# Kernel tuning notes

Hardware: AMD Instinct MI355X
Metric: run time of the kernel (lower is better)

## Reference

```python
import jax, jax.numpy as jnp
import numpy as np
import math

N_HEAD = 12
N_EMBD = 768

def setup_inputs() -> dict:
    key = jax.random.key(0)
    ks = jax.random.split(key, 5)
    B, T, C = 4, 2048, N_EMBD
    s_attn = 1.0 / math.sqrt(C)
    return {
        "x": jax.random.normal(ks[0], (B, T, C), jnp.float32),
        "w_attn": jax.random.normal(ks[1], (C, 3 * C), jnp.float32) * s_attn,
        "b_attn": jnp.zeros((3 * C,), jnp.float32),
        "w_proj": jax.random.normal(ks[2], (C, C), jnp.float32) * s_attn,
        "b_proj": jnp.zeros((C,), jnp.float32),
    }

def reference(x, w_attn, b_attn, w_proj, b_proj):
    B, T, C = x.shape
    H = N_HEAD
    D = C // H
    qkv = x @ w_attn + b_attn  # [B,T,3C]
    q, k, v = jnp.split(qkv, 3, axis=-1)
    # [B,T,C] -> [B,H,T,D]
    q = q.reshape(B, T, H, D).transpose(0, 2, 1, 3)
    k = k.reshape(B, T, H, D).transpose(0, 2, 1, 3)
    v = v.reshape(B, T, H, D).transpose(0, 2, 1, 3)
    att = jnp.einsum('bhqd,bhkd->bhqk', q, k) * (1.0 / math.sqrt(D))
    causal = jnp.tril(jnp.ones((T, T), bool))
    att = jnp.where(causal[None, None], att, -jnp.inf)
    att = jax.nn.softmax(att, axis=-1)
    y = jnp.einsum('bhqk,bhkd->bhqd', att, v)  # [B,H,T,D]
    y = y.transpose(0, 2, 1, 3).reshape(B, T, C)
    return y @ w_proj + b_proj
```

## Files before the change

kernel.cpp:

```cpp
#include <hip/hip_runtime.h>
#include <hip/hip_bf16.h>

typedef unsigned short u16;
typedef __attribute__((ext_vector_type(4))) short bf16x4;
typedef __attribute__((ext_vector_type(8))) short bf16x8;
typedef __attribute__((ext_vector_type(4))) float f32x4;
typedef __attribute__((ext_vector_type(16))) float f32x16;

#define NB_ 4
#define NT_ 2048
#define NC_ 768
#define NH_ 12
#define ND_ 64
#define NM_ (NB_*NT_)
#define KC_ 24

#define SCQ_ 0.18033688011112042f

__device__ __forceinline__ u16 f2bf(float f){
  union { float f; unsigned u; } c; c.f = f;
  unsigned u = c.u;
  return (u16)((u + 0x7fffu + ((u>>16)&1u)) >> 16);
}

__device__ __forceinline__ unsigned pkbf(float a, float b){
  __hip_bfloat162 h = __float22bfloat162_rn(make_float2(a,b));
  union { __hip_bfloat162 h; unsigned u; } c; c.h = h; return c.u;
}

__device__ __forceinline__ f32x16 mfma32(bf16x8 a, bf16x8 b, f32x16 c){
  return __builtin_amdgcn_mfma_f32_32x32x16_bf16(a, b, c, 0, 0, 0);
}

__device__ __forceinline__ void gload_lds16(const void* g, void* l){
  __builtin_amdgcn_global_load_lds(
    (const __attribute__((address_space(1))) void*)g,
    (__attribute__((address_space(3))) void*)l, 16, 0, 0);
}


__global__ __launch_bounds__(256) void cast_f32_bf16_k(
    const float* __restrict__ in, u16* __restrict__ out, int n4){
  int i = blockIdx.x*256 + threadIdx.x;
  if (i >= n4) return;
  float4 v = ((const float4*)in)[i];
  int row = i / (NC_/4), k4 = (i % (NC_/4))*4;
  size_t off = (((size_t)(row>>7)*KC_ + (k4>>5))*4 + ((k4>>3)&3))*1024 + (row&127)*8 + (k4&7);
  bf16x4 o;
  o[0]=(short)f2bf(v.x); o[1]=(short)f2bf(v.y);
  o[2]=(short)f2bf(v.z); o[3]=(short)f2bf(v.w);
  *(bf16x4*)(out + off) = o;
}

__global__ __launch_bounds__(256) void transpose_cast_k(
    const float* __restrict__ in, u16* __restrict__ out, int R, int Cc){
  __shared__ float tile[32][33];
  int tx = threadIdx.x, ty = threadIdx.y;
  int c0 = blockIdx.x*32, r0 = blockIdx.y*32;
  #pragma unroll
  for (int j=0;j<32;j+=8) tile[ty+j][tx] = in[(size_t)(r0+ty+j)*Cc + c0+tx];
  __syncthreads();
  #pragma unroll
  for (int j=0;j<32;j+=8){
    int n = c0+ty+j, k = r0+tx;
    size_t off = (((size_t)(n>>7)*KC_ + (k>>5))*4 + ((k>>3)&3))*1024 + (n&127)*8 + (k&7);
    out[off] = f2bf(tile[tx][ty+j]);
  }
}

template<int MODE>
__global__ __launch_bounds__(256,3) void gemm128p(
  const u16* __restrict__ A, const u16* __restrict__ BT, const float* __restrict__ bias,
  u16* __restrict__ qo, u16* __restrict__ ko, u16* __restrict__ vo,
  float* __restrict__ fo)
{
  __shared__ u16 lds[3][8192];
  const int t = threadIdx.x, w = t>>6, l = t&63;
  const int lq = l&31, h = l>>5;
  const int NXB = (MODE==0) ? 18 : 6;
  const int nwg = 64*NXB;
  int sw = (blockIdx.x & 7)*(nwg>>3) + (blockIdx.x >> 3);
  const int rb = sw / NXB, nb = sw % NXB;
  const int brow = rb*128, bcol = nb*128;
  const int wr = (w>>1)*64, wc = (w&1)*64;

  f32x16 acc[2][2];
  #pragma unroll
  for (int i=0;i<2;i++)
    #pragma unroll
    for (int j=0;j<2;j++)
      #pragma unroll
      for (int r=0;r<16;r++) acc[i][j][r] = 0.f;

  auto stage = [&](int buf, int kc){
    const u16* Ag = A  + ((size_t)(rb*KC_ + kc))*4096;
    const u16* Bg = BT + ((size_t)(nb*KC_ + kc))*4096;
    char* La = (char*)&lds[buf][0];
    char* Lb = (char*)&lds[buf][4096];
    #pragma unroll
    for (int it=0; it<2; ++it){
      gload_lds16(Ag + (it*256+t)*8, La + (it*256+t)*16);
      gload_lds16(Bg + (it*256+t)*8, Lb + (it*256+t)*16);
    }
  };

  stage(0,0);
  stage(1,1);
  int cur = 0;
  for (int kc=0; kc<KC_; ++kc){
    if (kc+1 < KC_) asm volatile("s_waitcnt vmcnt(4)\ns_barrier" ::: "memory");
    else            asm volatile("s_waitcnt vmcnt(0)\ns_barrier" ::: "memory");
    if (kc+2 < KC_){ int nb3 = cur+2; if (nb3>=3) nb3-=3; stage(nb3, kc+2); }
    const u16* La = &lds[cur][0];
    const u16* Lb = &lds[cur][4096];
    #pragma unroll
    for (int ks=0; ks<2; ++ks){
      bf16x8 af[2], bfr[2];
      #pragma unroll
      for (int mi=0;mi<2;mi++)
        af[mi]  = *(const bf16x8*)(La + ((2*ks+h)*128 + wr + mi*32 + lq)*8);
      #pragma unroll
      for (int nj=0;nj<2;nj++)
        bfr[nj] = *(const bf16x8*)(Lb + ((2*ks+h)*128 + wc + nj*32 + lq)*8);
      __builtin_amdgcn_s_setprio(1);
      #pragma unroll
      for (int mi=0;mi<2;mi++)
        #pragma unroll
        for (int nj=0;nj<2;nj++)
          acc[mi][nj] = mfma32(af[mi], bfr[nj], acc[mi][nj]);
      __builtin_amdgcn_s_setprio(0);
    }
    if (++cur == 3) cur = 0;
  }

  if (MODE == 1){
    #pragma unroll
    for (int nj=0;nj<2;nj++){
      int n = bcol + wc + nj*32 + lq;
      float bs = bias[n];
      #pragma unroll
      for (int mi=0;mi<2;mi++)
        #pragma unroll
        for (int r=0;r<16;r++){
          int m = brow + wr + mi*32 + (r&3) + 8*(r>>2) + 4*h;
          fo[(size_t)m*NC_ + n] = acc[mi][nj][r] + bs;
        }
    }
  } else {
    const int sec = nb/6;
    u16* outp = (sec==0) ? qo : (sec==1 ? ko : vo);
    #pragma unroll
    for (int nj=0;nj<2;nj++){
      int n = bcol + wc + nj*32 + lq;
      int cc = n - sec*NC_;
      int hd = cc >> 6, d = cc & 63;
      float bs = bias[n];
      #pragma unroll
      for (int mi=0;mi<2;mi++)
        #pragma unroll
        for (int r=0;r<16;r++){
          int m = brow + wr + mi*32 + (r&3) + 8*(r>>2) + 4*h;
          int bb = m >> 11, tt = m & 2047;
          float v = acc[mi][nj][r] + bs;
          if (sec == 0) v *= SCQ_;
          size_t bhbase = ((size_t)bb*NH_ + hd)*((size_t)NT_*ND_);
          size_t off;
          if (sec == 0){
            off = bhbase + (size_t)tt*ND_ + d;
          } else if (sec == 1){
            off = bhbase + (size_t)(tt>>6)*4096 + (size_t)(d>>3)*512 + (tt&63)*8 + (d&7);
          } else {
            int p = (tt & ~15) | (h<<3) | (r&3) | (((r>>2)&1)<<2);
            off = bhbase + (size_t)(p>>6)*4096 + (size_t)((p&63)>>3)*512 + d*8 + (p&7);
          }
          outp[off] = f2bf(v);
        }
    }
  }
}

__global__ __launch_bounds__(256,4) void attn_kernel(
    const u16* __restrict__ qg, const u16* __restrict__ kg,
    const u16* __restrict__ vg, u16* __restrict__ y)
{
  __shared__ u16 lds[2][8192];
  const int t = threadIdx.x, w = t>>6, l = t&63;
  const int lq = l&31, h = l>>5;
  const int bid = blockIdx.x;
  const int qt = 15 - (bid/48);
  const int bh = bid % 48;
  const int bb = bh / NH_, hh = bh % NH_;
  const u16* qp = qg + (size_t)bh*NT_*ND_;
  const u16* kp = kg + (size_t)bh*NT_*ND_;
  const u16* vp = vg + (size_t)bh*ND_*NT_;
  const int qmin = qt*128 + w*32;
  const int q = qmin + lq;

  bf16x8 Qf[4];
  {
    const u16* qr = qp + (size_t)q*ND_ + 8*h;
    #pragma unroll
    for (int ks=0; ks<4; ++ks) Qf[ks] = *(const bf16x8*)(qr + ks*16);
  }

  f32x16 o0, o1;
  float psum[16];
  #pragma unroll
  for (int r=0;r<16;r++){ o0[r]=0.f; o1[r]=0.f; psum[r]=0.f; }
  const int nc = 2*qt + 2;

  auto stage = [&](int buf, int c){
    const u16* kc2 = kp + c*4096;
    const u16* vc2 = vp + c*4096;
    #pragma unroll
    for (int it=0; it<2; ++it){
      gload_lds16(kc2 + (it*256 + t)*8, (char*)&lds[buf][0]    + (it*256 + t)*16);
      gload_lds16(vc2 + (it*256 + t)*8, (char*)&lds[buf][4096] + (it*256 + t)*16);
    }
  };

  stage(0,0);
  int cur = 0;
  for (int c=0; c<nc; ++c){
    asm volatile("s_waitcnt vmcnt(0)\ns_barrier" ::: "memory");
    if (c+1 < nc) stage(cur^1, c+1);

    const u16* Kb = &lds[cur][0];
    const u16* Vb = &lds[cur][4096];
    const int kv0 = c*64;

    f32x16 s0, s1;
    #pragma unroll
    for (int r=0;r<16;r++){ s0[r]=0.f; s1[r]=0.f; }
    __builtin_amdgcn_s_setprio(1);
    #pragma unroll
    for (int ks=0; ks<4; ++ks){
      bf16x8 k0 = *(const bf16x8*)(Kb + ((2*ks+h)*64      + lq)*8);
      bf16x8 k1 = *(const bf16x8*)(Kb + ((2*ks+h)*64 + 32 + lq)*8);
      s0 = mfma32(k0, Qf[ks], s0);
      s1 = mfma32(k1, Qf[ks], s1);
    }
    __builtin_amdgcn_s_setprio(0);

    if (kv0 + 63 > qmin){
      #pragma unroll
      for (int r=0;r<16;r++){
        int kva = kv0 + (r&3) + 8*(r>>2) + 4*h;
        s0[r] = (kva      <= q) ? s0[r] : -3e38f;
        s1[r] = (kva + 32 <= q) ? s1[r] : -3e38f;
      }
    }

    union { unsigned wd[16]; bf16x8 v[4]; } pf;
    #pragma unroll
    for (int j=0;j<8;j++){
      float a = exp2f(s0[2*j]), b = exp2f(s0[2*j+1]);
      psum[j] += a + b;
      pf.wd[j] = pkbf(a,b);
    }
    #pragma unroll
    for (int j=0;j<8;j++){
      float a = exp2f(s1[2*j]), b = exp2f(s1[2*j+1]);
      psum[8+j] += a + b;
      pf.wd[8+j] = pkbf(a,b);
    }

    __builtin_amdgcn_s_setprio(1);
    #pragma unroll
    for (int j=0;j<4;j++){
      bf16x8 v0 = *(const bf16x8*)(Vb + ((2*j+h)*64      + lq)*8);
      bf16x8 v1 = *(const bf16x8*)(Vb + ((2*j+h)*64 + 32 + lq)*8);
      o0 = mfma32(v0, pf.v[j], o0);
      o1 = mfma32(v1, pf.v[j], o1);
    }
    __builtin_amdgcn_s_setprio(0);
    cur ^= 1;
  }

  #pragma unroll
  for (int st=8; st>=1; st>>=1)
    #pragma unroll
    for (int i=0;i<st;i++) psum[i] += psum[i+st];
  float lsum = psum[0] + __shfl_xor(psum[0], 32);
  float inv = 1.f / lsum;

  const int m = bb*NT_ + q;
  const int rbm = m>>7, rr = m&127;
  #pragma unroll
  for (int db=0; db<2; ++db){
    #pragma unroll
    for (int g2=0; g2<4; ++g2){
      float e0 = (db ? o1[g2*4+0] : o0[g2*4+0]) * inv;
      float e1 = (db ? o1[g2*4+1] : o0[g2*4+1]) * inv;
      float e2 = (db ? o1[g2*4+2] : o0[g2*4+2]) * inv;
      float e3 = (db ? o1[g2*4+3] : o0[g2*4+3]) * inv;
      unsigned w0 = pkbf(e0,e1), w1 = pkbf(e2,e3);
      int k = hh*ND_ + db*32 + g2*8 + 4*h;
      size_t off = (((size_t)rbm*KC_ + (k>>5))*4 + ((k>>3)&3))*1024 + rr*8 + (k&7);
      *(uint2*)(y + off) = make_uint2(w0, w1);
    }
  }
}

extern "C" void kernel_launch(void* const* d_in, const int* in_sizes, int n_in,
                              void* d_out, int out_size, void* d_ws, size_t ws_size,
                              hipStream_t stream) {
  const float* x  = (const float*)d_in[0];
  const float* wa = (const float*)d_in[1];
  const float* ba = (const float*)d_in[2];
  const float* wp = (const float*)d_in[3];
  const float* bp = (const float*)d_in[4];
  float* out = (float*)d_out;

  char* ws = (char*)d_ws;
  const size_t szXB = (size_t)NM_*NC_*2;
  const size_t szWA = (size_t)3*NC_*NC_*2;
  const size_t szWP = (size_t)NC_*NC_*2;
  const size_t szQ  = szXB;
  u16* xb  = (u16*)(ws);
  u16* wat = (u16*)(ws + szXB);
  u16* wpt = (u16*)(ws + szXB + szWA);
  u16* qb  = (u16*)(ws + szXB + szWA + szWP);
  u16* kb  = (u16*)((char*)qb + szQ);
  u16* vb  = (u16*)((char*)kb + szQ);
  u16* yb  = xb;

  cast_f32_bf16_k<<<dim3((NM_*NC_/4 + 255)/256), dim3(256), 0, stream>>>(x, xb, NM_*NC_/4);
  transpose_cast_k<<<dim3(3*NC_/32, NC_/32), dim3(32,8), 0, stream>>>(wa, wat, NC_, 3*NC_);
  transpose_cast_k<<<dim3(NC_/32, NC_/32), dim3(32,8), 0, stream>>>(wp, wpt, NC_, NC_);
  gemm128p<0><<<dim3(64*18), dim3(256), 0, stream>>>(xb, wat, ba, qb, kb, vb, (float*)nullptr);
  attn_kernel<<<dim3(NB_*NH_*(NT_/128)), dim3(256), 0, stream>>>(qb, kb, vb, yb);
  gemm128p<1><<<dim3(64*6), dim3(256), 0, stream>>>(yb, wpt, bp,
      (u16*)nullptr, (u16*)nullptr, (u16*)nullptr, out);
}
```

Before: 132.9 us.

## Retile QKV GEMM to 256x96, double-buffer GEMMs, skip masked attention chunks

The QKV projection GEMM now uses 256x96 tiles (768 workgroups, one per CU-friendly grid) with a matching 96-wide weight panel layout, and both GEMMs move from triple to double buffering. The attention kernel skips fully masked KV chunks per wave and computes the softmax row sum with an extra MFMA against a ones vector instead of scalar adds plus shuffles. Together these aim to improve tile reuse and wave balance, cut wasted causal work, and trim VALU pressure, at the cost of less prefetch depth in the GEMMs and one extra MFMA per chunk in attention.

```diff
diff --git a/kernel.cpp b/kernel.cpp
--- a/kernel.cpp
+++ b/kernel.cpp
@@ -4,7 +4,6 @@
 typedef unsigned short u16;
 typedef __attribute__((ext_vector_type(4))) short bf16x4;
 typedef __attribute__((ext_vector_type(8))) short bf16x8;
-typedef __attribute__((ext_vector_type(4))) float f32x4;
 typedef __attribute__((ext_vector_type(16))) float f32x16;
 
 #define NB_ 4
@@ -52,6 +51,7 @@
   *(bf16x4*)(out + off) = o;
 }
 
+template<int PAN>
 __global__ __launch_bounds__(256) void transpose_cast_k(
     const float* __restrict__ in, u16* __restrict__ out, int R, int Cc){
   __shared__ float tile[32][33];
@@ -63,24 +63,112 @@
   #pragma unroll
   for (int j=0;j<32;j+=8){
     int n = c0+ty+j, k = r0+tx;
-    size_t off = (((size_t)(n>>7)*KC_ + (k>>5))*4 + ((k>>3)&3))*1024 + (n&127)*8 + (k&7);
+    size_t off = ((size_t)(n/PAN)*KC_ + (k>>5))*(PAN*32)
+               + (size_t)((k>>3)&3)*(PAN*8) + (n%PAN)*8 + (k&7);
     out[off] = f2bf(tile[tx][ty+j]);
   }
 }
 
-template<int MODE>
-__global__ __launch_bounds__(256,3) void gemm128p(
+__global__ __launch_bounds__(256,3) void gemmQ(
   const u16* __restrict__ A, const u16* __restrict__ BT, const float* __restrict__ bias,
-  u16* __restrict__ qo, u16* __restrict__ ko, u16* __restrict__ vo,
+  u16* __restrict__ qo, u16* __restrict__ ko, u16* __restrict__ vo)
+{
+  __shared__ u16 lds[2][11264];
+  const int t = threadIdx.x, w = t>>6, l = t&63;
+  const int lq = l&31, h = l>>5;
+  int sw = (blockIdx.x & 7)*96 + (blockIdx.x >> 3);
+  const int rb = sw / 24, nb = sw % 24;
+  const int brow = rb*256, bcol = nb*96;
+
+  f32x16 acc[2][3];
+  #pragma unroll
+  for (int i=0;i<2;i++)
+    #pragma unroll
+    for (int j=0;j<3;j++)
+      #pragma unroll
+      for (int r=0;r<16;r++) acc[i][j][r] = 0.f;
+
+  auto stage = [&](int buf, int kc){
+    const u16* A0 = A  + ((size_t)((rb*2  )*KC_ + kc))*4096;
+    const u16* A1 = A  + ((size_t)((rb*2+1)*KC_ + kc))*4096;
+    const u16* Bg = BT + ((size_t)(nb*KC_ + kc))*3072;
+    char* L = (char*)&lds[buf][0];
+    gload_lds16(A0 + t*8,         L + t*16);
+    gload_lds16(A0 + (256+t)*8,   L + (256+t)*16);
+    gload_lds16(A1 + t*8,         L + 8192  + t*16);
+    gload_lds16(A1 + (256+t)*8,   L + 8192  + (256+t)*16);
+    gload_lds16(Bg + t*8,         L + 16384 + t*16);
+    if (t < 128)
+      gload_lds16(Bg + (256+t)*8, L + 16384 + (256+t)*16);
+  };
+
+  stage(0,0);
+  int cur = 0;
+  for (int kc=0; kc<KC_; ++kc){
+    asm volatile("s_waitcnt vmcnt(0)\ns_barrier" ::: "memory");
+    if (kc+1 < KC_) stage(cur^1, kc+1);
+    const u16* La = &lds[cur][(w>>1)*4096];
+    const u16* Lb = &lds[cur][8192];
+    #pragma unroll
+    for (int ks=0; ks<2; ++ks){
+      bf16x8 af[2], bfr[3];
+      #pragma unroll
+      for (int mi=0;mi<2;mi++)
+        af[mi]  = *(const bf16x8*)(La + ((2*ks+h)*128 + (w&1)*64 + mi*32 + lq)*8);
+      #pragma unroll
+      for (int nj=0;nj<3;nj++)
+        bfr[nj] = *(const bf16x8*)(Lb + ((2*ks+h)*96 + nj*32 + lq)*8);
+      __builtin_amdgcn_s_setprio(1);
+      #pragma unroll
+      for (int mi=0;mi<2;mi++)
+        #pragma unroll
+        for (int nj=0;nj<3;nj++)
+          acc[mi][nj] = mfma32(af[mi], bfr[nj], acc[mi][nj]);
+      __builtin_amdgcn_s_setprio(0);
+    }
+    cur ^= 1;
+  }
+
+  const int sec = nb >> 3;
+  u16* outp = (sec==0) ? qo : (sec==1 ? ko : vo);
+  #pragma unroll
+  for (int nj=0;nj<3;nj++){
+    int n = bcol + nj*32 + lq;
+    int cc = n - sec*NC_;
+    int hd = cc >> 6, d = cc & 63;
+    float bs = bias[n];
+    #pragma unroll
+    for (int mi=0;mi<2;mi++)
+      #pragma unroll
+      for (int r=0;r<16;r++){
+        int m = brow + w*64 + mi*32 + (r&3) + 8*(r>>2) + 4*h;
+        int bb = m >> 11, tt = m & 2047;
+        float v = acc[mi][nj][r] + bs;
+        if (sec == 0) v *= SCQ_;
+        size_t bhbase = ((size_t)bb*NH_ + hd)*((size_t)NT_*ND_);
+        size_t off;
+        if (sec == 0){
+          off = bhbase + (size_t)tt*ND_ + d;
+        } else if (sec == 1){
+          off = bhbase + (size_t)(tt>>6)*4096 + (size_t)(d>>3)*512 + (tt&63)*8 + (d&7);
+        } else {
+          int p = (tt & ~15) | (h<<3) | (r&3) | (((r>>2)&1)<<2);
+          off = bhbase + (size_t)(p>>6)*4096 + (size_t)((p&63)>>3)*512 + d*8 + (p&7);
+        }
+        outp[off] = f2bf(v);
+      }
+  }
+}
+
+__global__ __launch_bounds__(256,4) void gemmP(
+  const u16* __restrict__ A, const u16* __restrict__ BT, const float* __restrict__ bias,
   float* __restrict__ fo)
 {
-  __shared__ u16 lds[3][8192];
+  __shared__ u16 lds[2][8192];
   const int t = threadIdx.x, w = t>>6, l = t&63;
   const int lq = l&31, h = l>>5;
-  const int NXB = (MODE==0) ? 18 : 6;
-  const int nwg = 64*NXB;
-  int sw = (blockIdx.x & 7)*(nwg>>3) + (blockIdx.x >> 3);
-  const int rb = sw / NXB, nb = sw % NXB;
+  int sw = (blockIdx.x & 7)*48 + (blockIdx.x >> 3);
+  const int rb = sw / 6, nb = sw % 6;
   const int brow = rb*128, bcol = nb*128;
   const int wr = (w>>1)*64, wc = (w&1)*64;
 
@@ -105,12 +193,10 @@
   };
 
   stage(0,0);
-  stage(1,1);
   int cur = 0;
   for (int kc=0; kc<KC_; ++kc){
-    if (kc+1 < KC_) asm volatile("s_waitcnt vmcnt(4)\ns_barrier" ::: "memory");
-    else            asm volatile("s_waitcnt vmcnt(0)\ns_barrier" ::: "memory");
-    if (kc+2 < KC_){ int nb3 = cur+2; if (nb3>=3) nb3-=3; stage(nb3, kc+2); }
+    asm volatile("s_waitcnt vmcnt(0)\ns_barrier" ::: "memory");
+    if (kc+1 < KC_) stage(cur^1, kc+1);
     const u16* La = &lds[cur][0];
     const u16* Lb = &lds[cur][4096];
     #pragma unroll
@@ -130,52 +216,20 @@
           acc[mi][nj] = mfma32(af[mi], bfr[nj], acc[mi][nj]);
       __builtin_amdgcn_s_setprio(0);
     }
-    if (++cur == 3) cur = 0;
-  }
-
-  if (MODE == 1){
-    #pragma unroll
-    for (int nj=0;nj<2;nj++){
-      int n = bcol + wc + nj*32 + lq;
-      float bs = bias[n];
-      #pragma unroll
-      for (int mi=0;mi<2;mi++)
-        #pragma unroll
-        for (int r=0;r<16;r++){
-          int m = brow + wr + mi*32 + (r&3) + 8*(r>>2) + 4*h;
-          fo[(size_t)m*NC_ + n] = acc[mi][nj][r] + bs;
-        }
-    }
-  } else {
-    const int sec = nb/6;
-    u16* outp = (sec==0) ? qo : (sec==1 ? ko : vo);
-    #pragma unroll
-    for (int nj=0;nj<2;nj++){
-      int n = bcol + wc + nj*32 + lq;
-      int cc = n - sec*NC_;
-      int hd = cc >> 6, d = cc & 63;
-      float bs = bias[n];
-      #pragma unroll
-      for (int mi=0;mi<2;mi++)
-        #pragma unroll
-        for (int r=0;r<16;r++){
-          int m = brow + wr + mi*32 + (r&3) + 8*(r>>2) + 4*h;
-          int bb = m >> 11, tt = m & 2047;
-          float v = acc[mi][nj][r] + bs;
-          if (sec == 0) v *= SCQ_;
-          size_t bhbase = ((size_t)bb*NH_ + hd)*((size_t)NT_*ND_);
-          size_t off;
-          if (sec == 0){
-            off = bhbase + (size_t)tt*ND_ + d;
-          } else if (sec == 1){
-            off = bhbase + (size_t)(tt>>6)*4096 + (size_t)(d>>3)*512 + (tt&63)*8 + (d&7);
-          } else {
-            int p = (tt & ~15) | (h<<3) | (r&3) | (((r>>2)&1)<<2);
-            off = bhbase + (size_t)(p>>6)*4096 + (size_t)((p&63)>>3)*512 + d*8 + (p&7);
-          }
-          outp[off] = f2bf(v);
-        }
-    }
+    cur ^= 1;
+  }
+
+  #pragma unroll
+  for (int nj=0;nj<2;nj++){
+    int n = bcol + wc + nj*32 + lq;
+    float bs = bias[n];
+    #pragma unroll
+    for (int mi=0;mi<2;mi++)
+      #pragma unroll
+      for (int r=0;r<16;r++){
+        int m = brow + wr + mi*32 + (r&3) + 8*(r>>2) + 4*h;
+        fo[(size_t)m*NC_ + n] = acc[mi][nj][r] + bs;
+      }
   }
 }
 
@@ -202,11 +256,13 @@
     #pragma unroll
     for (int ks=0; ks<4; ++ks) Qf[ks] = *(const bf16x8*)(qr + ks*16);
   }
-
-  f32x16 o0, o1;
-  float psum[16];
-  #pragma unroll
-  for (int r=0;r<16;r++){ o0[r]=0.f; o1[r]=0.f; psum[r]=0.f; }
+  bf16x8 ones;
+  #pragma unroll
+  for (int i=0;i<8;i++) ones[i] = (short)0x3F80;
+
+  f32x16 o0, o1, ls;
+  #pragma unroll
+  for (int r=0;r<16;r++){ o0[r]=0.f; o1[r]=0.f; ls[r]=0.f; }
   const int nc = 2*qt + 2;
 
   auto stage = [&](int buf, int c){
@@ -225,64 +281,56 @@
     asm volatile("s_waitcnt vmcnt(0)\ns_barrier" ::: "memory");
     if (c+1 < nc) stage(cur^1, c+1);
 
-    const u16* Kb = &lds[cur][0];
-    const u16* Vb = &lds[cur][4096];
     const int kv0 = c*64;
-
-    f32x16 s0, s1;
-    #pragma unroll
-    for (int r=0;r<16;r++){ s0[r]=0.f; s1[r]=0.f; }
-    __builtin_amdgcn_s_setprio(1);
-    #pragma unroll
-    for (int ks=0; ks<4; ++ks){
-      bf16x8 k0 = *(const bf16x8*)(Kb + ((2*ks+h)*64      + lq)*8);
-      bf16x8 k1 = *(const bf16x8*)(Kb + ((2*ks+h)*64 + 32 + lq)*8);
-      s0 = mfma32(k0, Qf[ks], s0);
-      s1 = mfma32(k1, Qf[ks], s1);
-    }
-    __builtin_amdgcn_s_setprio(0);
-
-    if (kv0 + 63 > qmin){
-      #pragma unroll
-      for (int r=0;r<16;r++){
-        int kva = kv0 + (r&3) + 8*(r>>2) + 4*h;
-        s0[r] = (kva      <= q) ? s0[r] : -3e38f;
-        s1[r] = (kva + 32 <= q) ? s1[r] : -3e38f;
-      }
-    }
-
-    union { unsigned wd[16]; bf16x8 v[4]; } pf;
-    #pragma unroll
-    for (int j=0;j<8;j++){
-      float a = exp2f(s0[2*j]), b = exp2f(s0[2*j+1]);
-      psum[j] += a + b;
-      pf.wd[j] = pkbf(a,b);
-    }
-    #pragma unroll
-    for (int j=0;j<8;j++){
-      float a = exp2f(s1[2*j]), b = exp2f(s1[2*j+1]);
-      psum[8+j] += a + b;
-      pf.wd[8+j] = pkbf(a,b);
-    }
-
-    __builtin_amdgcn_s_setprio(1);
-    #pragma unroll
-    for (int j=0;j<4;j++){
-      bf16x8 v0 = *(const bf16x8*)(Vb + ((2*j+h)*64      + lq)*8);
-      bf16x8 v1 = *(const bf16x8*)(Vb + ((2*j+h)*64 + 32 + lq)*8);
-      o0 = mfma32(v0, pf.v[j], o0);
-      o1 = mfma32(v1, pf.v[j], o1);
-    }
-    __builtin_amdgcn_s_setprio(0);
+    if (kv0 <= qmin + 31){
+      const u16* Kb = &lds[cur][0];
+      const u16* Vb = &lds[cur][4096];
+
+      f32x16 s0, s1;
+      #pragma unroll
+      for (int r=0;r<16;r++){ s0[r]=0.f; s1[r]=0.f; }
+      __builtin_amdgcn_s_setprio(1);
+      #pragma unroll
+      for (int ks=0; ks<4; ++ks){
+        bf16x8 k0 = *(const bf16x8*)(Kb + ((2*ks+h)*64      + lq)*8);
+        bf16x8 k1 = *(const bf16x8*)(Kb + ((2*ks+h)*64 + 32 + lq)*8);
+        s0 = mfma32(k0, Qf[ks], s0);
+        s1 = mfma32(k1, Qf[ks], s1);
+      }
+      __builtin_amdgcn_s_setprio(0);
+
+      if (kv0 + 63 > qmin){
+        #pragma unroll
+        for (int r=0;r<16;r++){
+          int kva = kv0 + (r&3) + 8*(r>>2) + 4*h;
+          s0[r] = (kva      <= q) ? s0[r] : -3e38f;
+          s1[r] = (kva + 32 <= q) ? s1[r] : -3e38f;
+        }
+      }
+
+      union { unsigned wd[16]; bf16x8 v[4]; } pf;
+      #pragma unroll
+      for (int j=0;j<8;j++)
+        pf.wd[j]   = pkbf(exp2f(s0[2*j]), exp2f(s0[2*j+1]));
+      #pragma unroll
+      for (int j=0;j<8;j++)
+        pf.wd[8+j] = pkbf(exp2f(s1[2*j]), exp2f(s1[2*j+1]));
+
+      __builtin_amdgcn_s_setprio(1);
+      #pragma unroll
+      for (int j=0;j<4;j++){
+        bf16x8 v0 = *(const bf16x8*)(Vb + ((2*j+h)*64      + lq)*8);
+        bf16x8 v1 = *(const bf16x8*)(Vb + ((2*j+h)*64 + 32 + lq)*8);
+        o0 = mfma32(v0, pf.v[j], o0);
+        o1 = mfma32(v1, pf.v[j], o1);
+        ls = mfma32(ones, pf.v[j], ls);
+      }
+      __builtin_amdgcn_s_setprio(0);
+    }
     cur ^= 1;
   }
 
-  #pragma unroll
-  for (int st=8; st>=1; st>>=1)
-    #pragma unroll
-    for (int i=0;i<st;i++) psum[i] += psum[i+st];
-  float lsum = psum[0] + __shfl_xor(psum[0], 32);
-  float inv = 1.f / lsum;
+  float inv = 1.f / ls[0];
 
   const int m = bb*NT_ + q;
   const int rbm = m>>7, rr = m&127;
@@ -326,10 +374,9 @@
   u16* yb  = xb;
 
   cast_f32_bf16_k<<<dim3((NM_*NC_/4 + 255)/256), dim3(256), 0, stream>>>(x, xb, NM_*NC_/4);
-  transpose_cast_k<<<dim3(3*NC_/32, NC_/32), dim3(32,8), 0, stream>>>(wa, wat, NC_, 3*NC_);
-  transpose_cast_k<<<dim3(NC_/32, NC_/32), dim3(32,8), 0, stream>>>(wp, wpt, NC_, NC_);
-  gemm128p<0><<<dim3(64*18), dim3(256), 0, stream>>>(xb, wat, ba, qb, kb, vb, (float*)nullptr);
+  transpose_cast_k<96><<<dim3(3*NC_/32, NC_/32), dim3(32,8), 0, stream>>>(wa, wat, NC_, 3*NC_);
+  transpose_cast_k<128><<<dim3(NC_/32, NC_/32), dim3(32,8), 0, stream>>>(wp, wpt, NC_, NC_);
+  gemmQ<<<dim3(768), dim3(256), 0, stream>>>(xb, wat, ba, qb, kb, vb);
   attn_kernel<<<dim3(NB_*NH_*(NT_/128)), dim3(256), 0, stream>>>(qb, kb, vb, yb);
-  gemm128p<1><<<dim3(64*6), dim3(256), 0, stream>>>(yb, wpt, bp,
-      (u16*)nullptr, (u16*)nullptr, (u16*)nullptr, out);
-}
+  gemmP<<<dim3(384), dim3(256), 0, stream>>>(yb, wpt, bp, out);
+}
```

Measured after the change: 131.8 us. No clear change (-0.8%).
